# Kernel tuning notes

Measured on AMD Instinct MI355X. Metric: run time of the kernel, lower is better.

The kernel has to match this reference:

```python
import jax, jax.numpy as jnp
import numpy as np

N = 50000       # nodes
E = 1600000     # edges (avg degree 32)
DIN = 128
DOUT = 128
EPS = 1e-5      # torch BatchNorm1d default eps


def setup_inputs() -> dict:
    key = jax.random.key(0)
    ks = jax.random.split(key, 6)
    x = jax.random.normal(ks[0], (N, DIN), dtype=jnp.float32)
    edge_index = jax.random.randint(ks[1], (2, E), 0, N, dtype=jnp.int32)
    edge_weight = jax.random.uniform(ks[2], (E,), dtype=jnp.float32)
    stdv = 1.0 / float(np.sqrt(DOUT))
    # main linear: uniform(-stdv, stdv) per reset_parameters
    W = jax.random.uniform(ks[3], (DOUT, DIN), dtype=jnp.float32, minval=-stdv, maxval=stdv)
    b = jnp.zeros((DOUT,), jnp.float32)
    # residual linear
    Wres = jax.random.uniform(ks[4], (DOUT, DIN), dtype=jnp.float32, minval=-stdv, maxval=stdv)
    bres = jnp.zeros((DOUT,), jnp.float32)
    # batchnorm affine params
    gamma = jnp.ones((DOUT,), jnp.float32)
    beta = jnp.zeros((DOUT,), jnp.float32)
    return {"x": x, "edge_index": edge_index, "edge_weight": edge_weight,
            "W": W, "b": b, "Wres": Wres, "bres": bres,
            "gamma": gamma, "beta": beta}


def reference(x, edge_index, edge_weight, W, b, Wres, bres, gamma, beta):
    # support = self.linear(x)
    support = x @ W.T + b                                   # [N, DOUT]
    # out = spmm(graph, support): out[d] = sum_e w_e * support[src_e] for dst_e == d
    src, dst = edge_index[0], edge_index[1]
    msgs = support[src] * edge_weight[:, None]              # [E, DOUT] gather
    out = jax.ops.segment_sum(msgs, dst, num_segments=N)    # [N, DOUT] scatter-add
    # batchnorm (training-mode batch statistics, biased variance)
    mean = jnp.mean(out, axis=0)
    var = jnp.var(out, axis=0)
    out = (out - mean) * jax.lax.rsqrt(var + EPS) * gamma + beta
    # relu
    out = jax.nn.relu(out)
    # residual projection of the input
    out = out + x @ Wres.T + bres
    return out
```

## Files before the change

kernel.cpp:

```cpp
#include <hip/hip_runtime.h>

#define DF 128
#define BN_EPS 1e-5f

typedef short s16x8 __attribute__((ext_vector_type(8)));
typedef float f32x4 __attribute__((ext_vector_type(4)));

__device__ __forceinline__ ushort f2b(float f) {
    uint u = __float_as_uint(f);
    u += 0x7fffu + ((u >> 16) & 1u);
    return (ushort)(u >> 16);
}
__device__ __forceinline__ float b2f_lo(uint v) { return __uint_as_float(v << 16); }
__device__ __forceinline__ float b2f_hi(uint v) { return __uint_as_float(v & 0xffff0000u); }

__global__ __launch_bounds__(256) void cvt_weights(
    const float* __restrict__ W, const float* __restrict__ Wres,
    ushort* __restrict__ Wcat)
{
    const int half = blockIdx.x >> 4;
    const float* src = half ? Wres : W;
    ushort* dstp = Wcat + half * 128 * DF;
    int t = (blockIdx.x & 15) * 256 + threadIdx.x;
    float4 v = reinterpret_cast<const float4*>(src)[t];
    ushort4 o;
    o.x = f2b(v.x); o.y = f2b(v.y); o.z = f2b(v.z); o.w = f2b(v.w);
    reinterpret_cast<ushort4*>(dstp)[t] = o;
}

__global__ __launch_bounds__(256) void gemm_mfma(
    const float* __restrict__ x, const ushort* __restrict__ Wcat,
    const float* __restrict__ b, const float* __restrict__ bres,
    ushort* __restrict__ support, float* __restrict__ res, int N)
{
    const int wave = threadIdx.x >> 6;
    const int lane = threadIdx.x & 63;
    const int base = (blockIdx.x * 4 + wave) * 32;
    if (base >= N) return;
    const int lrow = lane & 15;
    const int g4   = lane >> 4;
    const int koff = g4 * 8;
    const int row0 = base + lrow;
    const int row1 = base + 16 + lrow;
    const bool ok0 = row0 < N, ok1 = row1 < N;
    const int  a0r = ok0 ? row0 : (N - 1);
    const int  a1r = ok1 ? row1 : (N - 1);

    s16x8 xf0[4], xf1[4];
#pragma unroll
    for (int kb = 0; kb < 4; ++kb) {
        float4 f0 = reinterpret_cast<const float4*>(x)[(size_t)a0r * 32 + kb * 8 + g4 * 2];
        float4 f1 = reinterpret_cast<const float4*>(x)[(size_t)a0r * 32 + kb * 8 + g4 * 2 + 1];
        s16x8 v;
        v[0] = (short)f2b(f0.x); v[1] = (short)f2b(f0.y);
        v[2] = (short)f2b(f0.z); v[3] = (short)f2b(f0.w);
        v[4] = (short)f2b(f1.x); v[5] = (short)f2b(f1.y);
        v[6] = (short)f2b(f1.z); v[7] = (short)f2b(f1.w);
        xf0[kb] = v;
        float4 g0 = reinterpret_cast<const float4*>(x)[(size_t)a1r * 32 + kb * 8 + g4 * 2];
        float4 g1 = reinterpret_cast<const float4*>(x)[(size_t)a1r * 32 + kb * 8 + g4 * 2 + 1];
        s16x8 w;
        w[0] = (short)f2b(g0.x); w[1] = (short)f2b(g0.y);
        w[2] = (short)f2b(g0.z); w[3] = (short)f2b(g0.w);
        w[4] = (short)f2b(g1.x); w[5] = (short)f2b(g1.y);
        w[6] = (short)f2b(g1.z); w[7] = (short)f2b(g1.w);
        xf1[kb] = w;
    }

#pragma unroll
    for (int ct = 0; ct < 16; ++ct) {
        f32x4 acc0 = {0.f, 0.f, 0.f, 0.f};
        f32x4 acc1 = {0.f, 0.f, 0.f, 0.f};
#pragma unroll
        for (int kb = 0; kb < 4; ++kb) {
            s16x8 wf = *reinterpret_cast<const s16x8*>(
                &Wcat[(size_t)(ct * 16 + lrow) * 128 + kb * 32 + koff]);
            acc0 = __builtin_amdgcn_mfma_f32_16x16x32_bf16(wf, xf0[kb], acc0, 0, 0, 0);
            acc1 = __builtin_amdgcn_mfma_f32_16x16x32_bf16(wf, xf1[kb], acc1, 0, 0, 0);
        }
        int c0 = ct * 16 + 4 * g4;
        if (ct < 8) {
            float4 bias = *reinterpret_cast<const float4*>(&b[c0]);
            if (ok0) {
                ushort4 o;
                o.x = f2b(acc0[0] + bias.x); o.y = f2b(acc0[1] + bias.y);
                o.z = f2b(acc0[2] + bias.z); o.w = f2b(acc0[3] + bias.w);
                *reinterpret_cast<ushort4*>(&support[(size_t)row0 * 128 + c0]) = o;
            }
            if (ok1) {
                ushort4 o;
                o.x = f2b(acc1[0] + bias.x); o.y = f2b(acc1[1] + bias.y);
                o.z = f2b(acc1[2] + bias.z); o.w = f2b(acc1[3] + bias.w);
                *reinterpret_cast<ushort4*>(&support[(size_t)row1 * 128 + c0]) = o;
            }
        } else {
            int c = c0 - 128;
            float4 bias = *reinterpret_cast<const float4*>(&bres[c]);
            if (ok0) {
                float4 o = make_float4(acc0[0] + bias.x, acc0[1] + bias.y,
                                       acc0[2] + bias.z, acc0[3] + bias.w);
                *reinterpret_cast<float4*>(&res[(size_t)row0 * 128 + c]) = o;
            }
            if (ok1) {
                float4 o = make_float4(acc1[0] + bias.x, acc1[1] + bias.y,
                                       acc1[2] + bias.z, acc1[3] + bias.w);
                *reinterpret_cast<float4*>(&res[(size_t)row1 * 128 + c]) = o;
            }
        }
    }
}

__global__ __launch_bounds__(512) void bin_count(
    const int* __restrict__ dst, int* __restrict__ bktcnt, int E)
{
    __shared__ int h[1024];
    const int tid = threadIdx.x;
    for (int i = tid; i < 1024; i += 512) h[i] = 0;
    __syncthreads();
    const int base = blockIdx.x * 4096;
#pragma unroll
    for (int k = 0; k < 2; ++k) {
        int i = base + k * 2048 + tid * 4;
        if (i + 3 < E) {
            int4 d = *reinterpret_cast<const int4*>(&dst[i]);
            atomicAdd(&h[d.x >> 6], 1);
            atomicAdd(&h[d.y >> 6], 1);
            atomicAdd(&h[d.z >> 6], 1);
            atomicAdd(&h[d.w >> 6], 1);
        } else {
            for (int j = 0; j < 4; ++j)
                if (i + j < E) atomicAdd(&h[dst[i + j] >> 6], 1);
        }
    }
    __syncthreads();
    for (int i = tid; i < 1024; i += 512)
        if (h[i]) atomicAdd(&bktcnt[i], h[i]);
}

__global__ __launch_bounds__(512) void bin_scan(
    const int* __restrict__ bktcnt, int* __restrict__ bktptr,
    int* __restrict__ bktcur, int NBKT, int E)
{
    __shared__ int s[1024];
    const int t = threadIdx.x;
    int v0 = (t < NBKT) ? bktcnt[t] : 0;
    int v1 = (t + 512 < NBKT) ? bktcnt[t + 512] : 0;
    s[t] = v0; s[t + 512] = v1;
    __syncthreads();
    for (int off = 1; off < 1024; off <<= 1) {
        int a0 = (t >= off) ? s[t - off] : 0;
        int a1 = (t + 512 >= off) ? s[t + 512 - off] : 0;
        __syncthreads();
        s[t] += a0; s[t + 512] += a1;
        __syncthreads();
    }
    if (t < NBKT)       { int e = s[t] - v0;       bktptr[t] = e;       bktcur[t] = e; }
    if (t + 512 < NBKT) { int e = s[t+512] - v1;   bktptr[t+512] = e;   bktcur[t+512] = e; }
    if (t == 0) bktptr[NBKT] = E;
}

__global__ __launch_bounds__(512) void bin_scatter(
    const int* __restrict__ src, const int* __restrict__ dst,
    const float* __restrict__ ew, int* __restrict__ bktcur,
    uint2* __restrict__ recs, int E)
{
    __shared__ int cntl[1024];
    __shared__ int scn[1024];
    __shared__ int lcur[1024];
    __shared__ int gbase[1024];
    __shared__ uint2 stage[2048];
    const int tid = threadIdx.x;
    for (int i = tid; i < 1024; i += 512) cntl[i] = 0;
    __syncthreads();
    const int base = blockIdx.x * 2048;
    int myd[4];
#pragma unroll
    for (int k = 0; k < 4; ++k) {
        int i = base + k * 512 + tid;
        myd[k] = (i < E) ? dst[i] : -1;
        if (myd[k] >= 0) atomicAdd(&cntl[myd[k] >> 6], 1);
    }
    __syncthreads();
#pragma unroll
    for (int j = 0; j < 2; ++j) scn[tid + j * 512] = cntl[tid + j * 512];
    __syncthreads();
    for (int off = 1; off < 1024; off <<= 1) {
        int a[2];
#pragma unroll
        for (int j = 0; j < 2; ++j) {
            int idx = tid + j * 512;
            a[j] = (idx >= off) ? scn[idx - off] : 0;
        }
        __syncthreads();
#pragma unroll
        for (int j = 0; j < 2; ++j) scn[tid + j * 512] += a[j];
        __syncthreads();
    }
#pragma unroll
    for (int j = 0; j < 2; ++j) {
        int idx = tid + j * 512;
        int ex = scn[idx] - cntl[idx];
        scn[idx] = ex;
        lcur[idx] = ex;
    }
    for (int i = tid; i < 1024; i += 512) {
        int c = cntl[i];
        gbase[i] = c ? atomicAdd(&bktcur[i], c) : 0;
    }
    __syncthreads();
#pragma unroll
    for (int k = 0; k < 4; ++k) {
        int i = base + k * 512 + tid;
        if (i < E) {
            int d = myd[k];
            int bb = d >> 6;
            int p = atomicAdd(&lcur[bb], 1);
            uint w0 = (uint)src[i] | ((uint)(d & 63) << 16) | ((uint)bb << 22);
            stage[p] = make_uint2(w0, __float_as_uint(ew[i]));
        }
    }
    __syncthreads();
    const int nloc = min(2048, E - base);
    for (int j = tid; j < nloc; j += 512) {
        uint2 r = stage[j];
        int bb = r.x >> 22;
        int pos = gbase[bb] + (j - scn[bb]);
        recs[pos] = make_uint2(r.x & 0x3fffffu, r.y);
    }
}

__global__ __launch_bounds__(512) void spmm_sorted(
    const ushort* __restrict__ supportb, const uint2* __restrict__ recs,
    const int* __restrict__ bktptr, float* __restrict__ agg,
    float* __restrict__ bnacc, int N)
{
    __shared__ uint2 sorted[2048];
    __shared__ int hcnt[32];
    __shared__ int hoff[32];
    __shared__ int hcur[32];

    const int tid  = threadIdx.x;
    const int wv   = tid >> 6;
    const int lane = tid & 63;
    const int b    = blockIdx.x >> 1;
    const int half = blockIdx.x & 1;
    const int beg  = bktptr[b], end = bktptr[b + 1];
    const uint* sup = reinterpret_cast<const uint*>(supportb);

    float ax[4], ay[4];
#pragma unroll
    for (int r = 0; r < 4; ++r) { ax[r] = 0.f; ay[r] = 0.f; }

    for (int cbeg = beg; cbeg < end; cbeg += 2048) {
        const int cn = min(2048, end - cbeg);
        if (tid < 32) hcnt[tid] = 0;
        __syncthreads();
        uint2 myr[4];
        bool  mv[4];
#pragma unroll
        for (int u = 0; u < 4; ++u) {
            int j = tid + u * 512;
            mv[u] = false;
            if (j < cn) {
                myr[u] = recs[cbeg + j];
                int dl = (myr[u].x >> 16) & 63;
                if ((dl >> 5) == half) {
                    mv[u] = true;
                    atomicAdd(&hcnt[dl & 31], 1);
                }
            }
        }
        __syncthreads();
        if (tid < 32) {
            int v = hcnt[tid];
            int inc = v;
#pragma unroll
            for (int off = 1; off < 32; off <<= 1) {
                int t = __shfl_up(inc, off, 32);
                if (tid >= off) inc += t;
            }
            hoff[tid] = inc - v;
            hcur[tid] = inc - v;
        }
        __syncthreads();
#pragma unroll
        for (int u = 0; u < 4; ++u) {
            if (mv[u]) {
                int r = (myr[u].x >> 16) & 31;
                int p = atomicAdd(&hcur[r], 1);
                sorted[p] = myr[u];
            }
        }
        __syncthreads();
#pragma unroll
        for (int rr = 0; rr < 4; ++rr) {
            const int r  = wv * 4 + rr;
            const int s0 = hoff[r];
            const int s1 = s0 + hcnt[r];
            int k = s0;
            for (; k + 8 <= s1; k += 8) {
                uint2 e0 = sorted[k],   e1 = sorted[k+1], e2 = sorted[k+2], e3 = sorted[k+3];
                uint2 e4 = sorted[k+4], e5 = sorted[k+5], e6 = sorted[k+6], e7 = sorted[k+7];
                uint v0 = sup[(size_t)(e0.x & 0xffffu) * 64 + lane];
                uint v1 = sup[(size_t)(e1.x & 0xffffu) * 64 + lane];
                uint v2 = sup[(size_t)(e2.x & 0xffffu) * 64 + lane];
                uint v3 = sup[(size_t)(e3.x & 0xffffu) * 64 + lane];
                uint v4 = sup[(size_t)(e4.x & 0xffffu) * 64 + lane];
                uint v5 = sup[(size_t)(e5.x & 0xffffu) * 64 + lane];
                uint v6 = sup[(size_t)(e6.x & 0xffffu) * 64 + lane];
                uint v7 = sup[(size_t)(e7.x & 0xffffu) * 64 + lane];
                float w0 = __uint_as_float(e0.y), w1 = __uint_as_float(e1.y);
                float w2 = __uint_as_float(e2.y), w3 = __uint_as_float(e3.y);
                float w4 = __uint_as_float(e4.y), w5 = __uint_as_float(e5.y);
                float w6 = __uint_as_float(e6.y), w7 = __uint_as_float(e7.y);
                ax[rr] = fmaf(b2f_lo(v0), w0, ax[rr]); ay[rr] = fmaf(b2f_hi(v0), w0, ay[rr]);
                ax[rr] = fmaf(b2f_lo(v1), w1, ax[rr]); ay[rr] = fmaf(b2f_hi(v1), w1, ay[rr]);
                ax[rr] = fmaf(b2f_lo(v2), w2, ax[rr]); ay[rr] = fmaf(b2f_hi(v2), w2, ay[rr]);
                ax[rr] = fmaf(b2f_lo(v3), w3, ax[rr]); ay[rr] = fmaf(b2f_hi(v3), w3, ay[rr]);
                ax[rr] = fmaf(b2f_lo(v4), w4, ax[rr]); ay[rr] = fmaf(b2f_hi(v4), w4, ay[rr]);
                ax[rr] = fmaf(b2f_lo(v5), w5, ax[rr]); ay[rr] = fmaf(b2f_hi(v5), w5, ay[rr]);
                ax[rr] = fmaf(b2f_lo(v6), w6, ax[rr]); ay[rr] = fmaf(b2f_hi(v6), w6, ay[rr]);
                ax[rr] = fmaf(b2f_lo(v7), w7, ax[rr]); ay[rr] = fmaf(b2f_hi(v7), w7, ay[rr]);
            }
            for (; k + 4 <= s1; k += 4) {
                uint2 e0 = sorted[k], e1 = sorted[k+1], e2 = sorted[k+2], e3 = sorted[k+3];
                uint v0 = sup[(size_t)(e0.x & 0xffffu) * 64 + lane];
                uint v1 = sup[(size_t)(e1.x & 0xffffu) * 64 + lane];
                uint v2 = sup[(size_t)(e2.x & 0xffffu) * 64 + lane];
                uint v3 = sup[(size_t)(e3.x & 0xffffu) * 64 + lane];
                float w0 = __uint_as_float(e0.y), w1 = __uint_as_float(e1.y);
                float w2 = __uint_as_float(e2.y), w3 = __uint_as_float(e3.y);
                ax[rr] = fmaf(b2f_lo(v0), w0, ax[rr]); ay[rr] = fmaf(b2f_hi(v0), w0, ay[rr]);
                ax[rr] = fmaf(b2f_lo(v1), w1, ax[rr]); ay[rr] = fmaf(b2f_hi(v1), w1, ay[rr]);
                ax[rr] = fmaf(b2f_lo(v2), w2, ax[rr]); ay[rr] = fmaf(b2f_hi(v2), w2, ay[rr]);
                ax[rr] = fmaf(b2f_lo(v3), w3, ax[rr]); ay[rr] = fmaf(b2f_hi(v3), w3, ay[rr]);
            }
            for (; k < s1; ++k) {
                uint2 e = sorted[k];
                uint v = sup[(size_t)(e.x & 0xffffu) * 64 + lane];
                float w = __uint_as_float(e.y);
                ax[rr] = fmaf(b2f_lo(v), w, ax[rr]);
                ay[rr] = fmaf(b2f_hi(v), w, ay[rr]);
            }
        }
        __syncthreads();
    }

    const int row0 = b * 64 + half * 32 + wv * 4;
#pragma unroll
    for (int rr = 0; rr < 4; ++rr) {
        int gr = row0 + rr;
        if (gr < N)
            reinterpret_cast<float2*>(agg)[(size_t)gr * 64 + lane] = make_float2(ax[rr], ay[rr]);
    }

    float s1x = 0.f, s1y = 0.f, s2x = 0.f, s2y = 0.f;
#pragma unroll
    for (int rr = 0; rr < 4; ++rr) {
        s1x += ax[rr]; s1y += ay[rr];
        s2x = fmaf(ax[rr], ax[rr], s2x);
        s2y = fmaf(ay[rr], ay[rr], s2y);
    }
    float* red = reinterpret_cast<float*>(sorted);
    red[wv * 256 + 2 * lane]            = s1x;
    red[wv * 256 + 2 * lane + 1]        = s1y;
    red[2048 + wv * 256 + 2 * lane]     = s2x;
    red[2048 + wv * 256 + 2 * lane + 1] = s2y;
    __syncthreads();
    if (tid < 128) {
        float t1 = 0.f, t2 = 0.f;
#pragma unroll
        for (int w8 = 0; w8 < 8; ++w8) {
            t1 += red[w8 * 256 + tid];
            t2 += red[2048 + w8 * 256 + tid];
        }
        unsafeAtomicAdd(&bnacc[tid], t1);
        unsafeAtomicAdd(&bnacc[128 + tid], t2);
    }
}

__global__ __launch_bounds__(256) void bn_apply(
    const float* __restrict__ agg, const float* __restrict__ bnacc,
    const float* __restrict__ gamma, const float* __restrict__ beta,
    float* __restrict__ out, float invN, long total4)
{
    __shared__ float s_sc[128], s_sh[128];
    const int tid = threadIdx.x;
    if (tid < 128) {
        float mean = bnacc[tid] * invN;
        float var  = bnacc[128 + tid] * invN - mean * mean;
        float sc   = gamma[tid] * rsqrtf(var + BN_EPS);
        s_sc[tid] = sc;
        s_sh[tid] = beta[tid] - mean * sc;
    }
    __syncthreads();
    long t = (long)blockIdx.x * 256 + tid;
    if (t >= total4) return;
    int f4 = (int)(t & 31);
    float4 v  = reinterpret_cast<const float4*>(agg)[t];
    float4 sc = reinterpret_cast<const float4*>(s_sc)[f4];
    float4 sh = reinterpret_cast<const float4*>(s_sh)[f4];
    float4 r  = reinterpret_cast<float4*>(out)[t];
    float4 o;
    o.x = fmaxf(fmaf(v.x, sc.x, sh.x), 0.f) + r.x;
    o.y = fmaxf(fmaf(v.y, sc.y, sh.y), 0.f) + r.y;
    o.z = fmaxf(fmaf(v.z, sc.z, sh.z), 0.f) + r.z;
    o.w = fmaxf(fmaf(v.w, sc.w, sh.w), 0.f) + r.w;
    reinterpret_cast<float4*>(out)[t] = o;
}

extern "C" void kernel_launch(void* const* d_in, const int* in_sizes, int n_in,
                              void* d_out, int out_size, void* d_ws, size_t ws_size,
                              hipStream_t stream)
{
    const float* x     = (const float*)d_in[0];
    const int*   ei    = (const int*)  d_in[1];
    const float* ew    = (const float*)d_in[2];
    const float* W     = (const float*)d_in[3];
    const float* b     = (const float*)d_in[4];
    const float* Wres  = (const float*)d_in[5];
    const float* bres  = (const float*)d_in[6];
    const float* gamma = (const float*)d_in[7];
    const float* beta  = (const float*)d_in[8];

    const int N = in_sizes[0] / DF;
    const int E = in_sizes[2];
    const int* srci = ei;
    const int* dsti = ei + E;
    const int NBKT = (N + 63) >> 6;

    float*  fws      = (float*)d_ws;
    float*  agg      = fws;
    float*  bnacc    = agg + (size_t)N * DF;
    int*    bktcnt   = (int*)(bnacc + 256);
    int*    bktptr   = bktcnt + 1056;
    int*    bktcur   = bktptr + 1056;
    ushort* supportb = (ushort*)(bktcur + 1056);
    uint2*  recs     = (uint2*)(supportb + (size_t)N * DF);
    ushort* Wcat     = (ushort*)(recs + (size_t)E);
    float*  out      = (float*)d_out;

    hipMemsetAsync(bnacc, 0, (256 + 1056) * sizeof(float), stream);

    cvt_weights<<<32, 256, 0, stream>>>(W, Wres, Wcat);

    gemm_mfma<<<(N + 127) / 128, 256, 0, stream>>>(x, Wcat, b, bres, supportb, out, N);

    bin_count<<<(E + 4095) / 4096, 512, 0, stream>>>(dsti, bktcnt, E);
    bin_scan<<<1, 512, 0, stream>>>(bktcnt, bktptr, bktcur, NBKT, E);
    bin_scatter<<<(E + 2047) / 2048, 512, 0, stream>>>(srci, dsti, ew, bktcur, recs, E);

    spmm_sorted<<<NBKT * 2, 512, 0, stream>>>(supportb, recs, bktptr, agg, bnacc, N);

    long t4 = (long)N * (DF / 4);
    bn_apply<<<(int)((t4 + 255) / 256), 256, 0, stream>>>(
        agg, bnacc, gamma, beta, out, 1.0f / (float)N, t4);
}
```

Before: 252.6 us.

## Fuse weight conversion, bin count and scan; half-wave 8-byte gathers in SpMM

Weight conversion, bucket counting and the bucket prefix scan now run in one kernel, with a last-block-done counter triggering the scan. This removes two kernel launches and their gaps. The SpMM inner loop now has each half-wave handle alternate edges with 8-byte (4 bf16) gathers per lane, and the halves are combined with a cross-lane shuffle at the end. This doubles the edges in flight per wave but adds a shuffle reduction and an odd-tail special case.

```diff
diff --git a/kernel.cpp b/kernel.cpp
--- a/kernel.cpp
+++ b/kernel.cpp
@@ -14,18 +14,69 @@
 __device__ __forceinline__ float b2f_lo(uint v) { return __uint_as_float(v << 16); }
 __device__ __forceinline__ float b2f_hi(uint v) { return __uint_as_float(v & 0xffff0000u); }
 
-__global__ __launch_bounds__(256) void cvt_weights(
+__global__ __launch_bounds__(512) void prep(
     const float* __restrict__ W, const float* __restrict__ Wres,
-    ushort* __restrict__ Wcat)
-{
-    const int half = blockIdx.x >> 4;
-    const float* src = half ? Wres : W;
-    ushort* dstp = Wcat + half * 128 * DF;
-    int t = (blockIdx.x & 15) * 256 + threadIdx.x;
-    float4 v = reinterpret_cast<const float4*>(src)[t];
-    ushort4 o;
-    o.x = f2b(v.x); o.y = f2b(v.y); o.z = f2b(v.z); o.w = f2b(v.w);
-    reinterpret_cast<ushort4*>(dstp)[t] = o;
+    ushort* __restrict__ Wcat, const int* __restrict__ dst,
+    int* __restrict__ bktcnt, int* __restrict__ bktptr,
+    int* __restrict__ bktcur, int* __restrict__ donecnt,
+    int NBKT, int E, int nCnt)
+{
+    const int tid = threadIdx.x;
+    if (blockIdx.x < 16) {
+        const float* src = (blockIdx.x < 8) ? W : Wres;
+        ushort* dstp = Wcat + ((blockIdx.x < 8) ? 0 : 128 * DF);
+        int t = (int)(blockIdx.x & 7) * 512 + tid;
+        float4 v = reinterpret_cast<const float4*>(src)[t];
+        ushort4 o;
+        o.x = f2b(v.x); o.y = f2b(v.y); o.z = f2b(v.z); o.w = f2b(v.w);
+        reinterpret_cast<ushort4*>(dstp)[t] = o;
+        return;
+    }
+
+    __shared__ int h[1024];
+    const int cb = blockIdx.x - 16;
+    for (int i = tid; i < 1024; i += 512) h[i] = 0;
+    __syncthreads();
+    const int base = cb * 4096;
+#pragma unroll
+    for (int k = 0; k < 2; ++k) {
+        int i = base + k * 2048 + tid * 4;
+        if (i + 3 < E) {
+            int4 d = *reinterpret_cast<const int4*>(&dst[i]);
+            atomicAdd(&h[d.x >> 6], 1);
+            atomicAdd(&h[d.y >> 6], 1);
+            atomicAdd(&h[d.z >> 6], 1);
+            atomicAdd(&h[d.w >> 6], 1);
+        } else {
+            for (int j = 0; j < 4; ++j)
+                if (i + j < E) atomicAdd(&h[dst[i + j] >> 6], 1);
+        }
+    }
+    __syncthreads();
+    for (int i = tid; i < 1024; i += 512)
+        if (h[i]) atomicAdd(&bktcnt[i], h[i]);
+
+    __threadfence();
+    __shared__ int isLast;
+    if (tid == 0) isLast = (atomicAdd(donecnt, 1) == nCnt - 1) ? 1 : 0;
+    __syncthreads();
+    if (!isLast) return;
+    __threadfence();
+
+    int v0 = (tid < NBKT) ? bktcnt[tid] : 0;
+    int v1 = (tid + 512 < NBKT) ? bktcnt[tid + 512] : 0;
+    h[tid] = v0; h[tid + 512] = v1;
+    __syncthreads();
+    for (int off = 1; off < 1024; off <<= 1) {
+        int a0 = (tid >= off) ? h[tid - off] : 0;
+        int a1 = (tid + 512 >= off) ? h[tid + 512 - off] : 0;
+        __syncthreads();
+        h[tid] += a0; h[tid + 512] += a1;
+        __syncthreads();
+    }
+    if (tid < NBKT)       { int e = h[tid] - v0;       bktptr[tid] = e;       bktcur[tid] = e; }
+    if (tid + 512 < NBKT) { int e = h[tid + 512] - v1; bktptr[tid + 512] = e; bktcur[tid + 512] = e; }
+    if (tid == 0) bktptr[NBKT] = E;
 }
 
 __global__ __launch_bounds__(256) void gemm_mfma(
@@ -110,55 +161,6 @@
     }
 }
 
-__global__ __launch_bounds__(512) void bin_count(
-    const int* __restrict__ dst, int* __restrict__ bktcnt, int E)
-{
-    __shared__ int h[1024];
-    const int tid = threadIdx.x;
-    for (int i = tid; i < 1024; i += 512) h[i] = 0;
-    __syncthreads();
-    const int base = blockIdx.x * 4096;
-#pragma unroll
-    for (int k = 0; k < 2; ++k) {
-        int i = base + k * 2048 + tid * 4;
-        if (i + 3 < E) {
-            int4 d = *reinterpret_cast<const int4*>(&dst[i]);
-            atomicAdd(&h[d.x >> 6], 1);
-            atomicAdd(&h[d.y >> 6], 1);
-            atomicAdd(&h[d.z >> 6], 1);
-            atomicAdd(&h[d.w >> 6], 1);
-        } else {
-            for (int j = 0; j < 4; ++j)
-                if (i + j < E) atomicAdd(&h[dst[i + j] >> 6], 1);
-        }
-    }
-    __syncthreads();
-    for (int i = tid; i < 1024; i += 512)
-        if (h[i]) atomicAdd(&bktcnt[i], h[i]);
-}
-
-__global__ __launch_bounds__(512) void bin_scan(
-    const int* __restrict__ bktcnt, int* __restrict__ bktptr,
-    int* __restrict__ bktcur, int NBKT, int E)
-{
-    __shared__ int s[1024];
-    const int t = threadIdx.x;
-    int v0 = (t < NBKT) ? bktcnt[t] : 0;
-    int v1 = (t + 512 < NBKT) ? bktcnt[t + 512] : 0;
-    s[t] = v0; s[t + 512] = v1;
-    __syncthreads();
-    for (int off = 1; off < 1024; off <<= 1) {
-        int a0 = (t >= off) ? s[t - off] : 0;
-        int a1 = (t + 512 >= off) ? s[t + 512 - off] : 0;
-        __syncthreads();
-        s[t] += a0; s[t + 512] += a1;
-        __syncthreads();
-    }
-    if (t < NBKT)       { int e = s[t] - v0;       bktptr[t] = e;       bktcur[t] = e; }
-    if (t + 512 < NBKT) { int e = s[t+512] - v1;   bktptr[t+512] = e;   bktcur[t+512] = e; }
-    if (t == 0) bktptr[NBKT] = E;
-}
-
 __global__ __launch_bounds__(512) void bin_scatter(
     const int* __restrict__ src, const int* __restrict__ dst,
     const float* __restrict__ ew, int* __restrict__ bktcur,
@@ -229,6 +231,47 @@
     }
 }
 
+#define ACC(A, vv, ww) { \
+    A[0] = fmaf(b2f_lo((vv).x), (ww), A[0]); \
+    A[1] = fmaf(b2f_hi((vv).x), (ww), A[1]); \
+    A[2] = fmaf(b2f_lo((vv).y), (ww), A[2]); \
+    A[3] = fmaf(b2f_hi((vv).y), (ww), A[3]); }
+
+#define ROWLOOP(RR, A) { \
+    const int r_ = wv * 4 + RR; \
+    const int s0_ = hoff[r_]; \
+    const int s1_ = s0_ + hcnt[r_]; \
+    int k = s0_; \
+    for (; k + 16 <= s1_; k += 16) { \
+        uint2 e0 = sorted[k + hl],      e1 = sorted[k + 2 + hl]; \
+        uint2 e2 = sorted[k + 4 + hl],  e3 = sorted[k + 6 + hl]; \
+        uint2 e4 = sorted[k + 8 + hl],  e5 = sorted[k + 10 + hl]; \
+        uint2 e6 = sorted[k + 12 + hl], e7 = sorted[k + 14 + hl]; \
+        uint2 v0 = sup2[(size_t)(e0.x & 0xffffu) * 32 + cl]; \
+        uint2 v1 = sup2[(size_t)(e1.x & 0xffffu) * 32 + cl]; \
+        uint2 v2 = sup2[(size_t)(e2.x & 0xffffu) * 32 + cl]; \
+        uint2 v3 = sup2[(size_t)(e3.x & 0xffffu) * 32 + cl]; \
+        uint2 v4 = sup2[(size_t)(e4.x & 0xffffu) * 32 + cl]; \
+        uint2 v5 = sup2[(size_t)(e5.x & 0xffffu) * 32 + cl]; \
+        uint2 v6 = sup2[(size_t)(e6.x & 0xffffu) * 32 + cl]; \
+        uint2 v7 = sup2[(size_t)(e7.x & 0xffffu) * 32 + cl]; \
+        ACC(A, v0, __uint_as_float(e0.y)); ACC(A, v1, __uint_as_float(e1.y)); \
+        ACC(A, v2, __uint_as_float(e2.y)); ACC(A, v3, __uint_as_float(e3.y)); \
+        ACC(A, v4, __uint_as_float(e4.y)); ACC(A, v5, __uint_as_float(e5.y)); \
+        ACC(A, v6, __uint_as_float(e6.y)); ACC(A, v7, __uint_as_float(e7.y)); \
+    } \
+    for (; k + 2 <= s1_; k += 2) { \
+        uint2 e = sorted[k + hl]; \
+        uint2 v = sup2[(size_t)(e.x & 0xffffu) * 32 + cl]; \
+        ACC(A, v, __uint_as_float(e.y)); \
+    } \
+    if (k < s1_) { \
+        uint2 e = sorted[k]; \
+        uint2 v = sup2[(size_t)(e.x & 0xffffu) * 32 + cl]; \
+        float w = hl ? 0.f : __uint_as_float(e.y); \
+        ACC(A, v, w); \
+    } }
+
 __global__ __launch_bounds__(512) void spmm_sorted(
     const ushort* __restrict__ supportb, const uint2* __restrict__ recs,
     const int* __restrict__ bktptr, float* __restrict__ agg,
@@ -242,14 +285,17 @@
     const int tid  = threadIdx.x;
     const int wv   = tid >> 6;
     const int lane = tid & 63;
+    const int hl   = lane >> 5;
+    const int cl   = lane & 31;
     const int b    = blockIdx.x >> 1;
     const int half = blockIdx.x & 1;
     const int beg  = bktptr[b], end = bktptr[b + 1];
-    const uint* sup = reinterpret_cast<const uint*>(supportb);
-
-    float ax[4], ay[4];
-#pragma unroll
-    for (int r = 0; r < 4; ++r) { ax[r] = 0.f; ay[r] = 0.f; }
+    const uint2* sup2 = reinterpret_cast<const uint2*>(supportb);
+
+    f32x4 acc0 = {0.f, 0.f, 0.f, 0.f};
+    f32x4 acc1 = {0.f, 0.f, 0.f, 0.f};
+    f32x4 acc2 = {0.f, 0.f, 0.f, 0.f};
+    f32x4 acc3 = {0.f, 0.f, 0.f, 0.f};
 
     for (int cbeg = beg; cbeg < end; cbeg += 2048) {
         const int cn = min(2048, end - cbeg);
@@ -292,87 +338,43 @@
             }
         }
         __syncthreads();
-#pragma unroll
-        for (int rr = 0; rr < 4; ++rr) {
-            const int r  = wv * 4 + rr;
-            const int s0 = hoff[r];
-            const int s1 = s0 + hcnt[r];
-            int k = s0;
-            for (; k + 8 <= s1; k += 8) {
-                uint2 e0 = sorted[k],   e1 = sorted[k+1], e2 = sorted[k+2], e3 = sorted[k+3];
-                uint2 e4 = sorted[k+4], e5 = sorted[k+5], e6 = sorted[k+6], e7 = sorted[k+7];
-                uint v0 = sup[(size_t)(e0.x & 0xffffu) * 64 + lane];
-                uint v1 = sup[(size_t)(e1.x & 0xffffu) * 64 + lane];
-                uint v2 = sup[(size_t)(e2.x & 0xffffu) * 64 + lane];
-                uint v3 = sup[(size_t)(e3.x & 0xffffu) * 64 + lane];
-                uint v4 = sup[(size_t)(e4.x & 0xffffu) * 64 + lane];
-                uint v5 = sup[(size_t)(e5.x & 0xffffu) * 64 + lane];
-                uint v6 = sup[(size_t)(e6.x & 0xffffu) * 64 + lane];
-                uint v7 = sup[(size_t)(e7.x & 0xffffu) * 64 + lane];
-                float w0 = __uint_as_float(e0.y), w1 = __uint_as_float(e1.y);
-                float w2 = __uint_as_float(e2.y), w3 = __uint_as_float(e3.y);
-                float w4 = __uint_as_float(e4.y), w5 = __uint_as_float(e5.y);
-                float w6 = __uint_as_float(e6.y), w7 = __uint_as_float(e7.y);
-                ax[rr] = fmaf(b2f_lo(v0), w0, ax[rr]); ay[rr] = fmaf(b2f_hi(v0), w0, ay[rr]);
-                ax[rr] = fmaf(b2f_lo(v1), w1, ax[rr]); ay[rr] = fmaf(b2f_hi(v1), w1, ay[rr]);
-                ax[rr] = fmaf(b2f_lo(v2), w2, ax[rr]); ay[rr] = fmaf(b2f_hi(v2), w2, ay[rr]);
-                ax[rr] = fmaf(b2f_lo(v3), w3, ax[rr]); ay[rr] = fmaf(b2f_hi(v3), w3, ay[rr]);
-                ax[rr] = fmaf(b2f_lo(v4), w4, ax[rr]); ay[rr] = fmaf(b2f_hi(v4), w4, ay[rr]);
-                ax[rr] = fmaf(b2f_lo(v5), w5, ax[rr]); ay[rr] = fmaf(b2f_hi(v5), w5, ay[rr]);
-                ax[rr] = fmaf(b2f_lo(v6), w6, ax[rr]); ay[rr] = fmaf(b2f_hi(v6), w6, ay[rr]);
-                ax[rr] = fmaf(b2f_lo(v7), w7, ax[rr]); ay[rr] = fmaf(b2f_hi(v7), w7, ay[rr]);
-            }
-            for (; k + 4 <= s1; k += 4) {
-                uint2 e0 = sorted[k], e1 = sorted[k+1], e2 = sorted[k+2], e3 = sorted[k+3];
-                uint v0 = sup[(size_t)(e0.x & 0xffffu) * 64 + lane];
-                uint v1 = sup[(size_t)(e1.x & 0xffffu) * 64 + lane];
-                uint v2 = sup[(size_t)(e2.x & 0xffffu) * 64 + lane];
-                uint v3 = sup[(size_t)(e3.x & 0xffffu) * 64 + lane];
-                float w0 = __uint_as_float(e0.y), w1 = __uint_as_float(e1.y);
-                float w2 = __uint_as_float(e2.y), w3 = __uint_as_float(e3.y);
-                ax[rr] = fmaf(b2f_lo(v0), w0, ax[rr]); ay[rr] = fmaf(b2f_hi(v0), w0, ay[rr]);
-                ax[rr] = fmaf(b2f_lo(v1), w1, ax[rr]); ay[rr] = fmaf(b2f_hi(v1), w1, ay[rr]);
-                ax[rr] = fmaf(b2f_lo(v2), w2, ax[rr]); ay[rr] = fmaf(b2f_hi(v2), w2, ay[rr]);
-                ax[rr] = fmaf(b2f_lo(v3), w3, ax[rr]); ay[rr] = fmaf(b2f_hi(v3), w3, ay[rr]);
-            }
-            for (; k < s1; ++k) {
-                uint2 e = sorted[k];
-                uint v = sup[(size_t)(e.x & 0xffffu) * 64 + lane];
-                float w = __uint_as_float(e.y);
-                ax[rr] = fmaf(b2f_lo(v), w, ax[rr]);
-                ay[rr] = fmaf(b2f_hi(v), w, ay[rr]);
-            }
-        }
-        __syncthreads();
+        ROWLOOP(0, acc0)
+        ROWLOOP(1, acc1)
+        ROWLOOP(2, acc2)
+        ROWLOOP(3, acc3)
+        __syncthreads();
+    }
+
+#pragma unroll
+    for (int j = 0; j < 4; ++j) {
+        acc0[j] += __shfl_xor(acc0[j], 32, 64);
+        acc1[j] += __shfl_xor(acc1[j], 32, 64);
+        acc2[j] += __shfl_xor(acc2[j], 32, 64);
+        acc3[j] += __shfl_xor(acc3[j], 32, 64);
     }
 
     const int row0 = b * 64 + half * 32 + wv * 4;
-#pragma unroll
-    for (int rr = 0; rr < 4; ++rr) {
-        int gr = row0 + rr;
-        if (gr < N)
-            reinterpret_cast<float2*>(agg)[(size_t)gr * 64 + lane] = make_float2(ax[rr], ay[rr]);
-    }
-
-    float s1x = 0.f, s1y = 0.f, s2x = 0.f, s2y = 0.f;
-#pragma unroll
-    for (int rr = 0; rr < 4; ++rr) {
-        s1x += ax[rr]; s1y += ay[rr];
-        s2x = fmaf(ax[rr], ax[rr], s2x);
-        s2y = fmaf(ay[rr], ay[rr], s2y);
-    }
-    float* red = reinterpret_cast<float*>(sorted);
-    red[wv * 256 + 2 * lane]            = s1x;
-    red[wv * 256 + 2 * lane + 1]        = s1y;
-    red[2048 + wv * 256 + 2 * lane]     = s2x;
-    red[2048 + wv * 256 + 2 * lane + 1] = s2y;
+    if (hl == 0) {
+        if (row0 + 0 < N) *reinterpret_cast<f32x4*>(&agg[(size_t)(row0 + 0) * 128 + cl * 4]) = acc0;
+        if (row0 + 1 < N) *reinterpret_cast<f32x4*>(&agg[(size_t)(row0 + 1) * 128 + cl * 4]) = acc1;
+        if (row0 + 2 < N) *reinterpret_cast<f32x4*>(&agg[(size_t)(row0 + 2) * 128 + cl * 4]) = acc2;
+        if (row0 + 3 < N) *reinterpret_cast<f32x4*>(&agg[(size_t)(row0 + 3) * 128 + cl * 4]) = acc3;
+    }
+
+    f32x4 s1v = acc0 + acc1 + acc2 + acc3;
+    f32x4 s2v = acc0 * acc0 + acc1 * acc1 + acc2 * acc2 + acc3 * acc3;
+    float* redf = reinterpret_cast<float*>(sorted);
+    if (hl == 0) {
+        *reinterpret_cast<f32x4*>(&redf[wv * 128 + cl * 4]) = s1v;
+        *reinterpret_cast<f32x4*>(&redf[1024 + wv * 128 + cl * 4]) = s2v;
+    }
     __syncthreads();
     if (tid < 128) {
         float t1 = 0.f, t2 = 0.f;
 #pragma unroll
         for (int w8 = 0; w8 < 8; ++w8) {
-            t1 += red[w8 * 256 + tid];
-            t2 += red[2048 + w8 * 256 + tid];
+            t1 += redf[w8 * 128 + tid];
+            t2 += redf[1024 + w8 * 128 + tid];
         }
         unsafeAtomicAdd(&bnacc[tid], t1);
         unsafeAtomicAdd(&bnacc[128 + tid], t2);
@@ -433,21 +435,22 @@
     float*  agg      = fws;
     float*  bnacc    = agg + (size_t)N * DF;
     int*    bktcnt   = (int*)(bnacc + 256);
-    int*    bktptr   = bktcnt + 1056;
+    int*    donecnt  = bktcnt + 1056;
+    int*    bktptr   = donecnt + 32;
     int*    bktcur   = bktptr + 1056;
     ushort* supportb = (ushort*)(bktcur + 1056);
     uint2*  recs     = (uint2*)(supportb + (size_t)N * DF);
     ushort* Wcat     = (ushort*)(recs + (size_t)E);
     float*  out      = (float*)d_out;
 
-    hipMemsetAsync(bnacc, 0, (256 + 1056) * sizeof(float), stream);
-
-    cvt_weights<<<32, 256, 0, stream>>>(W, Wres, Wcat);
+    hipMemsetAsync(bnacc, 0, (256 + 1056 + 32) * sizeof(float), stream);
+
+    const int nCnt = (E + 4095) / 4096;
+    prep<<<16 + nCnt, 512, 0, stream>>>(W, Wres, Wcat, dsti, bktcnt, bktptr,
+                                        bktcur, donecnt, NBKT, E, nCnt);
 
     gemm_mfma<<<(N + 127) / 128, 256, 0, stream>>>(x, Wcat, b, bres, supportb, out, N);
 
-    bin_count<<<(E + 4095) / 4096, 512, 0, stream>>>(dsti, bktcnt, E);
-    bin_scan<<<1, 512, 0, stream>>>(bktcnt, bktptr, bktcur, NBKT, E);
     bin_scatter<<<(E + 2047) / 2048, 512, 0, stream>>>(srci, dsti, ew, bktcur, recs, E);
 
     spmm_sorted<<<NBKT * 2, 512, 0, stream>>>(supportb, recs, bktptr, agg, bnacc, N);
```

Result: slower. 306.0 us (+21.1%).

## Merge weight conversion with histogram and GEMM with bin scatter into combined launches

Applied to the files above, without the earlier changes.

Weight bf16 conversion is folded into the edge-histogram kernel as extra blocks. The MFMA GEMM now runs as leading blocks of the bin-scatter kernel, with 512-thread blocks of 8 waves. This removes two kernel launches and lets the independent GEMM and edge-binning work run concurrently on the GPU. The cost is that GEMM blocks now carry the scatter kernel's large shared-memory allocation, which may lower their occupancy.

```diff
diff --git a/kernel.cpp b/kernel.cpp
--- a/kernel.cpp
+++ b/kernel.cpp
@@ -14,110 +14,27 @@
 __device__ __forceinline__ float b2f_lo(uint v) { return __uint_as_float(v << 16); }
 __device__ __forceinline__ float b2f_hi(uint v) { return __uint_as_float(v & 0xffff0000u); }
 
-__global__ __launch_bounds__(256) void cvt_weights(
+__global__ __launch_bounds__(512) void prep(
     const float* __restrict__ W, const float* __restrict__ Wres,
-    ushort* __restrict__ Wcat)
-{
-    const int half = blockIdx.x >> 4;
-    const float* src = half ? Wres : W;
-    ushort* dstp = Wcat + half * 128 * DF;
-    int t = (blockIdx.x & 15) * 256 + threadIdx.x;
-    float4 v = reinterpret_cast<const float4*>(src)[t];
-    ushort4 o;
-    o.x = f2b(v.x); o.y = f2b(v.y); o.z = f2b(v.z); o.w = f2b(v.w);
-    reinterpret_cast<ushort4*>(dstp)[t] = o;
-}
-
-__global__ __launch_bounds__(256) void gemm_mfma(
-    const float* __restrict__ x, const ushort* __restrict__ Wcat,
-    const float* __restrict__ b, const float* __restrict__ bres,
-    ushort* __restrict__ support, float* __restrict__ res, int N)
-{
-    const int wave = threadIdx.x >> 6;
-    const int lane = threadIdx.x & 63;
-    const int base = (blockIdx.x * 4 + wave) * 32;
-    if (base >= N) return;
-    const int lrow = lane & 15;
-    const int g4   = lane >> 4;
-    const int koff = g4 * 8;
-    const int row0 = base + lrow;
-    const int row1 = base + 16 + lrow;
-    const bool ok0 = row0 < N, ok1 = row1 < N;
-    const int  a0r = ok0 ? row0 : (N - 1);
-    const int  a1r = ok1 ? row1 : (N - 1);
-
-    s16x8 xf0[4], xf1[4];
-#pragma unroll
-    for (int kb = 0; kb < 4; ++kb) {
-        float4 f0 = reinterpret_cast<const float4*>(x)[(size_t)a0r * 32 + kb * 8 + g4 * 2];
-        float4 f1 = reinterpret_cast<const float4*>(x)[(size_t)a0r * 32 + kb * 8 + g4 * 2 + 1];
-        s16x8 v;
-        v[0] = (short)f2b(f0.x); v[1] = (short)f2b(f0.y);
-        v[2] = (short)f2b(f0.z); v[3] = (short)f2b(f0.w);
-        v[4] = (short)f2b(f1.x); v[5] = (short)f2b(f1.y);
-        v[6] = (short)f2b(f1.z); v[7] = (short)f2b(f1.w);
-        xf0[kb] = v;
-        float4 g0 = reinterpret_cast<const float4*>(x)[(size_t)a1r * 32 + kb * 8 + g4 * 2];
-        float4 g1 = reinterpret_cast<const float4*>(x)[(size_t)a1r * 32 + kb * 8 + g4 * 2 + 1];
-        s16x8 w;
-        w[0] = (short)f2b(g0.x); w[1] = (short)f2b(g0.y);
-        w[2] = (short)f2b(g0.z); w[3] = (short)f2b(g0.w);
-        w[4] = (short)f2b(g1.x); w[5] = (short)f2b(g1.y);
-        w[6] = (short)f2b(g1.z); w[7] = (short)f2b(g1.w);
-        xf1[kb] = w;
-    }
-
-#pragma unroll
-    for (int ct = 0; ct < 16; ++ct) {
-        f32x4 acc0 = {0.f, 0.f, 0.f, 0.f};
-        f32x4 acc1 = {0.f, 0.f, 0.f, 0.f};
-#pragma unroll
-        for (int kb = 0; kb < 4; ++kb) {
-            s16x8 wf = *reinterpret_cast<const s16x8*>(
-                &Wcat[(size_t)(ct * 16 + lrow) * 128 + kb * 32 + koff]);
-            acc0 = __builtin_amdgcn_mfma_f32_16x16x32_bf16(wf, xf0[kb], acc0, 0, 0, 0);
-            acc1 = __builtin_amdgcn_mfma_f32_16x16x32_bf16(wf, xf1[kb], acc1, 0, 0, 0);
-        }
-        int c0 = ct * 16 + 4 * g4;
-        if (ct < 8) {
-            float4 bias = *reinterpret_cast<const float4*>(&b[c0]);
-            if (ok0) {
-                ushort4 o;
-                o.x = f2b(acc0[0] + bias.x); o.y = f2b(acc0[1] + bias.y);
-                o.z = f2b(acc0[2] + bias.z); o.w = f2b(acc0[3] + bias.w);
-                *reinterpret_cast<ushort4*>(&support[(size_t)row0 * 128 + c0]) = o;
-            }
-            if (ok1) {
-                ushort4 o;
-                o.x = f2b(acc1[0] + bias.x); o.y = f2b(acc1[1] + bias.y);
-                o.z = f2b(acc1[2] + bias.z); o.w = f2b(acc1[3] + bias.w);
-                *reinterpret_cast<ushort4*>(&support[(size_t)row1 * 128 + c0]) = o;
-            }
-        } else {
-            int c = c0 - 128;
-            float4 bias = *reinterpret_cast<const float4*>(&bres[c]);
-            if (ok0) {
-                float4 o = make_float4(acc0[0] + bias.x, acc0[1] + bias.y,
-                                       acc0[2] + bias.z, acc0[3] + bias.w);
-                *reinterpret_cast<float4*>(&res[(size_t)row0 * 128 + c]) = o;
-            }
-            if (ok1) {
-                float4 o = make_float4(acc1[0] + bias.x, acc1[1] + bias.y,
-                                       acc1[2] + bias.z, acc1[3] + bias.w);
-                *reinterpret_cast<float4*>(&res[(size_t)row1 * 128 + c]) = o;
-            }
-        }
-    }
-}
-
-__global__ __launch_bounds__(512) void bin_count(
-    const int* __restrict__ dst, int* __restrict__ bktcnt, int E)
-{
+    ushort* __restrict__ Wcat, const int* __restrict__ dst,
+    int* __restrict__ bktcnt, int E)
+{
+    const int tid = threadIdx.x;
+    if (blockIdx.x < 16) {
+        const float* src = (blockIdx.x < 8) ? W : Wres;
+        ushort* dstp = Wcat + ((blockIdx.x < 8) ? 0 : 128 * DF);
+        int t = (int)(blockIdx.x & 7) * 512 + tid;
+        float4 v = reinterpret_cast<const float4*>(src)[t];
+        ushort4 o;
+        o.x = f2b(v.x); o.y = f2b(v.y); o.z = f2b(v.z); o.w = f2b(v.w);
+        reinterpret_cast<ushort4*>(dstp)[t] = o;
+        return;
+    }
     __shared__ int h[1024];
-    const int tid = threadIdx.x;
+    const int cb = blockIdx.x - 16;
     for (int i = tid; i < 1024; i += 512) h[i] = 0;
     __syncthreads();
-    const int base = blockIdx.x * 4096;
+    const int base = cb * 4096;
 #pragma unroll
     for (int k = 0; k < 2; ++k) {
         int i = base + k * 2048 + tid * 4;
@@ -159,7 +76,10 @@
     if (t == 0) bktptr[NBKT] = E;
 }
 
-__global__ __launch_bounds__(512) void bin_scatter(
+__global__ __launch_bounds__(512) void gemm_scatter(
+    const float* __restrict__ x, const ushort* __restrict__ Wcat,
+    const float* __restrict__ b, const float* __restrict__ bres,
+    ushort* __restrict__ support, float* __restrict__ res, int N, int gemmB,
     const int* __restrict__ src, const int* __restrict__ dst,
     const float* __restrict__ ew, int* __restrict__ bktcur,
     uint2* __restrict__ recs, int E)
@@ -169,10 +89,92 @@
     __shared__ int lcur[1024];
     __shared__ int gbase[1024];
     __shared__ uint2 stage[2048];
+
     const int tid = threadIdx.x;
+
+    if ((int)blockIdx.x < gemmB) {
+        const int wave = tid >> 6;
+        const int lane = tid & 63;
+        const int base = ((int)blockIdx.x * 8 + wave) * 32;
+        if (base >= N) return;
+        const int lrow = lane & 15;
+        const int g4   = lane >> 4;
+        const int koff = g4 * 8;
+        const int row0 = base + lrow;
+        const int row1 = base + 16 + lrow;
+        const bool ok0 = row0 < N, ok1 = row1 < N;
+        const int  a0r = ok0 ? row0 : (N - 1);
+        const int  a1r = ok1 ? row1 : (N - 1);
+
+        s16x8 xf0[4], xf1[4];
+#pragma unroll
+        for (int kb = 0; kb < 4; ++kb) {
+            float4 f0 = reinterpret_cast<const float4*>(x)[(size_t)a0r * 32 + kb * 8 + g4 * 2];
+            float4 f1 = reinterpret_cast<const float4*>(x)[(size_t)a0r * 32 + kb * 8 + g4 * 2 + 1];
+            s16x8 v;
+            v[0] = (short)f2b(f0.x); v[1] = (short)f2b(f0.y);
+            v[2] = (short)f2b(f0.z); v[3] = (short)f2b(f0.w);
+            v[4] = (short)f2b(f1.x); v[5] = (short)f2b(f1.y);
+            v[6] = (short)f2b(f1.z); v[7] = (short)f2b(f1.w);
+            xf0[kb] = v;
+            float4 g0 = reinterpret_cast<const float4*>(x)[(size_t)a1r * 32 + kb * 8 + g4 * 2];
+            float4 g1 = reinterpret_cast<const float4*>(x)[(size_t)a1r * 32 + kb * 8 + g4 * 2 + 1];
+            s16x8 w;
+            w[0] = (short)f2b(g0.x); w[1] = (short)f2b(g0.y);
+            w[2] = (short)f2b(g0.z); w[3] = (short)f2b(g0.w);
+            w[4] = (short)f2b(g1.x); w[5] = (short)f2b(g1.y);
+            w[6] = (short)f2b(g1.z); w[7] = (short)f2b(g1.w);
+            xf1[kb] = w;
+        }
+
+#pragma unroll
+        for (int ct = 0; ct < 16; ++ct) {
+            f32x4 acc0 = {0.f, 0.f, 0.f, 0.f};
+            f32x4 acc1 = {0.f, 0.f, 0.f, 0.f};
+#pragma unroll
+            for (int kb = 0; kb < 4; ++kb) {
+                s16x8 wf = *reinterpret_cast<const s16x8*>(
+                    &Wcat[(size_t)(ct * 16 + lrow) * 128 + kb * 32 + koff]);
+                acc0 = __builtin_amdgcn_mfma_f32_16x16x32_bf16(wf, xf0[kb], acc0, 0, 0, 0);
+                acc1 = __builtin_amdgcn_mfma_f32_16x16x32_bf16(wf, xf1[kb], acc1, 0, 0, 0);
+            }
+            int c0 = ct * 16 + 4 * g4;
+            if (ct < 8) {
+                float4 bias = *reinterpret_cast<const float4*>(&b[c0]);
+                if (ok0) {
+                    ushort4 o;
+                    o.x = f2b(acc0[0] + bias.x); o.y = f2b(acc0[1] + bias.y);
+                    o.z = f2b(acc0[2] + bias.z); o.w = f2b(acc0[3] + bias.w);
+                    *reinterpret_cast<ushort4*>(&support[(size_t)row0 * 128 + c0]) = o;
+                }
+                if (ok1) {
+                    ushort4 o;
+                    o.x = f2b(acc1[0] + bias.x); o.y = f2b(acc1[1] + bias.y);
+                    o.z = f2b(acc1[2] + bias.z); o.w = f2b(acc1[3] + bias.w);
+                    *reinterpret_cast<ushort4*>(&support[(size_t)row1 * 128 + c0]) = o;
+                }
+            } else {
+                int c = c0 - 128;
+                float4 bias = *reinterpret_cast<const float4*>(&bres[c]);
+                if (ok0) {
+                    float4 o = make_float4(acc0[0] + bias.x, acc0[1] + bias.y,
+                                           acc0[2] + bias.z, acc0[3] + bias.w);
+                    *reinterpret_cast<float4*>(&res[(size_t)row0 * 128 + c]) = o;
+                }
+                if (ok1) {
+                    float4 o = make_float4(acc1[0] + bias.x, acc1[1] + bias.y,
+                                           acc1[2] + bias.z, acc1[3] + bias.w);
+                    *reinterpret_cast<float4*>(&res[(size_t)row1 * 128 + c]) = o;
+                }
+            }
+        }
+        return;
+    }
+
+    const int cb = (int)blockIdx.x - gemmB;
     for (int i = tid; i < 1024; i += 512) cntl[i] = 0;
     __syncthreads();
-    const int base = blockIdx.x * 2048;
+    const int base = cb * 2048;
     int myd[4];
 #pragma unroll
     for (int k = 0; k < 4; ++k) {
@@ -442,13 +444,16 @@
 
     hipMemsetAsync(bnacc, 0, (256 + 1056) * sizeof(float), stream);
 
-    cvt_weights<<<32, 256, 0, stream>>>(W, Wres, Wcat);
-
-    gemm_mfma<<<(N + 127) / 128, 256, 0, stream>>>(x, Wcat, b, bres, supportb, out, N);
-
-    bin_count<<<(E + 4095) / 4096, 512, 0, stream>>>(dsti, bktcnt, E);
+    const int nHist = (E + 4095) / 4096;
+    prep<<<16 + nHist, 512, 0, stream>>>(W, Wres, Wcat, dsti, bktcnt, E);
+
     bin_scan<<<1, 512, 0, stream>>>(bktcnt, bktptr, bktcur, NBKT, E);
-    bin_scatter<<<(E + 2047) / 2048, 512, 0, stream>>>(srci, dsti, ew, bktcur, recs, E);
+
+    const int gemmB = (N + 255) / 256;
+    const int scatB = (E + 2047) / 2048;
+    gemm_scatter<<<gemmB + scatB, 512, 0, stream>>>(
+        x, Wcat, b, bres, supportb, out, N, gemmB,
+        srci, dsti, ew, bktcur, recs, E);
 
     spmm_sorted<<<NBKT * 2, 512, 0, stream>>>(supportb, recs, bktptr, agg, bnacc, N);
 
```

Result: faster. 226.3 us (-10.4%).
